# Performance work log

Measured on AMD Instinct MI355X. Metric: run time of the kernel, lower is better.

## Reference

```python
import jax, jax.numpy as jnp
import numpy as np

N_V, N_E = 4096, 16384
IN_V, OUT_V, IN_E = 128, 128, 64


def setup_inputs() -> dict:
    key = jax.random.key(0)
    k1, k2, k3, k4, k5, k6, k7 = jax.random.split(key, 7)
    stdv = 1.0 / np.sqrt(OUT_V)
    return {
        "H_v": jax.random.normal(k1, (N_V, IN_V), dtype=jnp.float32),
        "H_e": jax.random.normal(k2, (N_E, IN_E), dtype=jnp.float32),
        "adj_e": jnp.zeros((1, 1), dtype=jnp.float32),  # unused in node_layer branch
        "adj_v": jax.random.uniform(k3, (N_V, N_V), dtype=jnp.float32),
        "T": jax.random.uniform(k4, (N_V, N_E), dtype=jnp.float32),
        "weight": jax.random.uniform(k5, (IN_V, OUT_V), minval=-stdv, maxval=stdv, dtype=jnp.float32),
        "p": jax.random.normal(k6, (1, IN_E), dtype=jnp.float32),
        "bias": jax.random.uniform(k7, (OUT_V,), minval=-stdv, maxval=stdv, dtype=jnp.float32),
    }


def reference(H_v, H_e, adj_e, adj_v, T, weight, p, bias):
    # node_layer=True branch of AlternateConvolution.forward
    # diag((H_e @ p.T).T[0]) -> per-edge scalar; T @ diag(d) == column-scale T
    diag_vals = (H_e @ p.T)[:, 0]                      # [n_e]
    multiplier1 = (T * diag_vals[None, :]) @ T.T       # [n_v, n_v]
    eye = jnp.eye(multiplier1.shape[0], dtype=multiplier1.dtype)
    M1 = eye + (1.0 - eye) * multiplier1               # diagonal forced to 1
    adjusted_A = M1 * adj_v                            # elementwise adjacency mask
    ret = adjusted_A @ (H_v @ weight) + bias           # [n_v, out_v]
    return (ret, H_e)
```

## Files before the change

kernel.cpp:

```cpp
#include <hip/hip_runtime.h>
#include <stdint.h>


typedef __attribute__((ext_vector_type(4))) float floatx4;
typedef __attribute__((ext_vector_type(4))) int intx4;
typedef __attribute__((ext_vector_type(16))) int intx16;
typedef __attribute__((ext_vector_type(8))) short short8;
typedef __attribute__((ext_vector_type(4))) unsigned short u16x4;

#define AS1 __attribute__((address_space(1)))
#define AS3 __attribute__((address_space(3)))

__device__ __forceinline__ void gload_lds16(const void* g, void* l) {
  __builtin_amdgcn_global_load_lds(
      (const AS1 unsigned int*)(uintptr_t)g,
      (AS3 unsigned int*)(uint32_t)(uintptr_t)l, 16, 0, 0);
}

__device__ __forceinline__ unsigned short f32_to_bf16(float f) {
  union { float f; unsigned int u; } v;
  v.f = f;
  unsigned int r = 0x7fffu + ((v.u >> 16) & 1u);
  return (unsigned short)((v.u + r) >> 16);
}

__device__ __forceinline__ float bf16_to_f32(unsigned short s) {
  union { unsigned int u; float f; } cv;
  cv.u = (unsigned int)s << 16;
  return cv.f;
}

__device__ __forceinline__ void tri_decode(int t, int& bi, int& bj) {
  bi = 0;
  while (t >= 32 - bi) { t -= 32 - bi; ++bi; }
  bj = bi + t;
}

#define TA_SCALE 3.96875f
#define DEQ_SCALE (32.0f / 16129.0f)

__global__ __launch_bounds__(256) void edge_dot_kernel(
    const float* __restrict__ He, const float* __restrict__ p,
    float* __restrict__ dvals) {
  int e = blockIdx.x * 4 + (threadIdx.x >> 6);
  int lane = threadIdx.x & 63;
  float v = He[e * 64 + lane] * p[lane];
#pragma unroll
  for (int off = 32; off > 0; off >>= 1) v += __shfl_down(v, off);
  if (lane == 0) dvals[e] = v;
}

__global__ __launch_bounds__(256) void copy4_kernel(
    const floatx4* __restrict__ src, floatx4* __restrict__ dst, int n4) {
  int i = blockIdx.x * 256 + threadIdx.x;
  if (i < n4)
    __builtin_nontemporal_store(__builtin_nontemporal_load(src + i), dst + i);
}

__global__ __launch_bounds__(256) void convert_T_i8_kernel(
    const floatx4* __restrict__ T4, const float* __restrict__ dvals,
    uint2* __restrict__ Ta8, uint2* __restrict__ Tb8) {
  int i = blockIdx.x * 256 + threadIdx.x;
  floatx4 t0 = __builtin_nontemporal_load(T4 + 2 * i);
  floatx4 t1 = __builtin_nontemporal_load(T4 + 2 * i + 1);
  int col = (i << 3) & 16383;
  const floatx4* dv = (const floatx4*)(dvals + col);
  floatx4 d0 = dv[0], d1 = dv[1];
  union { signed char c[8]; uint2 u; } qa, qb;
#pragma unroll
  for (int q = 0; q < 4; ++q) {
    float sa0 = fminf(fmaxf(t0[q] * d0[q] * TA_SCALE, -127.f), 127.f);
    float sa1 = fminf(fmaxf(t1[q] * d1[q] * TA_SCALE, -127.f), 127.f);
    qa.c[q]     = (signed char)(int)rintf(sa0);
    qa.c[q + 4] = (signed char)(int)rintf(sa1);
    qb.c[q]     = (signed char)(int)rintf(t0[q] * 127.0f);
    qb.c[q + 4] = (signed char)(int)rintf(t1[q] * 127.0f);
  }
  Ta8[i] = qa.u;
  Tb8[i] = qb.u;
}

__global__ __launch_bounds__(256) void hwt_kernel(
    const float* __restrict__ Hv, const float* __restrict__ W,
    unsigned short* __restrict__ HWT) {
  int idx = blockIdx.x * 256 + threadIdx.x;
  int j = idx & 4095, o = idx >> 12;
  float s = 0.f;
#pragma unroll 8
  for (int c = 0; c < 128; ++c) s += Hv[j * 128 + c] * W[c * 128 + o];
  HWT[o * 4096 + j] = f32_to_bf16(s);
}

__global__ __launch_bounds__(256) void gemm1_split_kernel(
    const signed char* __restrict__ Ta, const signed char* __restrict__ Tb,
    int* __restrict__ part) {
  constexpr int K = 16384;
  __shared__ __align__(16) signed char As[2][128 * 128];
  __shared__ __align__(16) signed char Bs[2][128 * 128];

  const int d = blockIdx.x;
  const int rank = (d & 7) * 132 + (d >> 3);
  const int h = rank >= 528 ? 1 : 0;
  const int t = rank - h * 528;
  int bi, bj;
  tri_decode(t, bi, bj);

  const int tid = threadIdx.x;
  const int wave = tid >> 6, lane = tid & 63;
  const int wr = (wave >> 1) * 64, wc = (wave & 1) * 64;
  const int row32 = lane & 31, khalf = lane >> 5;

  const int srow = tid >> 3;
  const int cg = (tid & 7) ^ (srow & 7);
  const signed char* Ag = Ta + (size_t)(bi * 128 + srow) * K + cg * 16;
  const signed char* Bg = Tb + (size_t)(bj * 128 + srow) * K + cg * 16;

  intx16 acc[2][2] = {};

  const int kbeg = h * 8192, kend = kbeg + 8192;

  auto stage = [&](int b, int k0) {
#pragma unroll
    for (int q = 0; q < 4; ++q) {
      gload_lds16(Ag + (size_t)(q * 32) * K + k0, &As[b][q * 4096 + tid * 16]);
      gload_lds16(Bg + (size_t)(q * 32) * K + k0, &Bs[b][q * 4096 + tid * 16]);
    }
  };

  auto compute = [&](int b) {
    intx4 af[2][4], bf[2][4];
#pragma unroll
    for (int x = 0; x < 2; ++x) {
      const int ra = wr + x * 32 + row32;
      const int rb = wc + x * 32 + row32;
#pragma unroll
      for (int sk = 0; sk < 4; ++sk) {
        af[x][sk] =
            *(const intx4*)&As[b][ra * 128 + ((sk * 2 + khalf) ^ (ra & 7)) * 16];
        bf[x][sk] =
            *(const intx4*)&Bs[b][rb * 128 + ((sk * 2 + khalf) ^ (rb & 7)) * 16];
      }
    }
#pragma unroll
    for (int sk = 0; sk < 4; ++sk)
#pragma unroll
      for (int tr = 0; tr < 2; ++tr)
#pragma unroll
        for (int tc = 0; tc < 2; ++tc)
          acc[tr][tc] = __builtin_amdgcn_mfma_i32_32x32x32_i8(
              af[tr][sk], bf[tc][sk], acc[tr][tc], 0, 0, 0);
  };

  stage(0, kbeg);
  __syncthreads();
  int buf = 0;
  for (int k0 = kbeg; k0 < kend - 128; k0 += 128) {
    stage(buf ^ 1, k0 + 128);
    compute(buf);
    __syncthreads();
    buf ^= 1;
  }
  compute(buf);

  int* pt = part + ((size_t)h * 528 + t) * 16384;
#pragma unroll
  for (int tr = 0; tr < 2; ++tr)
#pragma unroll
    for (int tc = 0; tc < 2; ++tc) {
      const int col = wc + tc * 32 + row32;
#pragma unroll
      for (int r = 0; r < 16; ++r) {
        const int row = wr + tr * 32 + (r & 3) + 8 * (r >> 2) + 4 * khalf;
        __builtin_nontemporal_store(acc[tr][tc][r], &pt[row * 128 + col]);
      }
    }
}

__global__ __launch_bounds__(256) void combine_kernel(
    const int* __restrict__ part, const float* __restrict__ adj_v,
    unsigned short* __restrict__ adjA) {
  constexpr int NV = 4096;
  __shared__ unsigned short mt[128 * 68];

  const int b = blockIdx.x;
  const int t = b >> 1, r0 = (b & 1) * 64;
  int bi, bj;
  tri_decode(t, bi, bj);
  const int tid = threadIdx.x;
  const bool diag = (bi == bj);

  const int* pt0 = part + (size_t)t * 16384;
  const int* pt1 = pt0 + (size_t)528 * 16384;

#pragma unroll
  for (int j = 0; j < 8; ++j) {
    const int e = j * 1024 + tid * 4;
    const int row = r0 + (e >> 7);
    const int col = e & 127;
    intx4 a = __builtin_nontemporal_load((const intx4*)(pt0 + row * 128 + col));
    intx4 c = __builtin_nontemporal_load((const intx4*)(pt1 + row * 128 + col));
    floatx4 msk = __builtin_nontemporal_load(
        (const floatx4*)(adj_v + (size_t)(bi * 128 + row) * NV + bj * 128 + col));
    u16x4 o;
#pragma unroll
    for (int q = 0; q < 4; ++q) {
      float m = (float)(a[q] + c[q]) * DEQ_SCALE;
      float val = (diag && row == col + q) ? msk[q] : m * msk[q];
      ((unsigned short*)&o)[q] = f32_to_bf16(val);
      if (!diag) mt[(col + q) * 68 + (row - r0)] = f32_to_bf16(m);
    }
    *(u16x4*)(adjA + (size_t)(bi * 128 + row) * NV + bj * 128 + col) = o;
  }

  if (diag) return;
  __syncthreads();

#pragma unroll
  for (int j = 0; j < 8; ++j) {
    const int e = j * 1024 + tid * 4;
    const int mc = e >> 6;
    const int mr = e & 63;
    u16x4 mv = *(const u16x4*)&mt[mc * 68 + mr];
    floatx4 msk = __builtin_nontemporal_load(
        (const floatx4*)(adj_v + (size_t)(bj * 128 + mc) * NV + bi * 128 + r0 + mr));
    u16x4 o;
#pragma unroll
    for (int q = 0; q < 4; ++q)
      ((unsigned short*)&o)[q] =
          f32_to_bf16(bf16_to_f32(((const unsigned short*)&mv)[q]) * msk[q]);
    *(u16x4*)(adjA + (size_t)(bj * 128 + mc) * NV + bi * 128 + r0 + mr) = o;
  }
}

__global__ __launch_bounds__(256) void gemm2_kernel(
    const unsigned short* __restrict__ adjA, const unsigned short* __restrict__ HWT,
    float* __restrict__ gpart) {
  constexpr int K = 4096, OUTV = 128;
  __shared__ __align__(16) unsigned short As[2][128 * 32];
  __shared__ __align__(16) unsigned short Bs[2][128 * 32];

  const int tid = threadIdx.x;
  const int wave = tid >> 6, lane = tid & 63;
  const int bi = blockIdx.x, ks = blockIdx.y;
  const int wr = (wave >> 1) * 64, wc = (wave & 1) * 64;
  const int quad = lane >> 4, mrow = lane & 15;

  const int sr = tid >> 2, sc = (tid & 3) * 8;
  const unsigned short* Ag = adjA + (size_t)(bi * 128 + sr) * K + sc;
  const unsigned short* Bg = HWT + (size_t)sr * K + sc;

  floatx4 acc[4][4] = {};

  const int kbeg = ks * 512, kend = kbeg + 512;

  auto stage = [&](int b, int k0) {
    gload_lds16(Ag + k0, &As[b][tid * 8]);
    gload_lds16(Ag + (size_t)64 * K + k0, &As[b][tid * 8 + 2048]);
    gload_lds16(Bg + k0, &Bs[b][tid * 8]);
    gload_lds16(Bg + (size_t)64 * K + k0, &Bs[b][tid * 8 + 2048]);
  };

  auto compute = [&](int b) {
    short8 af[4], bf[4];
#pragma unroll
    for (int x = 0; x < 4; ++x) {
      af[x] = *(const short8*)&As[b][(wr + x * 16 + mrow) * 32 + quad * 8];
      bf[x] = *(const short8*)&Bs[b][(wc + x * 16 + mrow) * 32 + quad * 8];
    }
#pragma unroll
    for (int tr = 0; tr < 4; ++tr)
#pragma unroll
      for (int tc = 0; tc < 4; ++tc)
        acc[tr][tc] = __builtin_amdgcn_mfma_f32_16x16x32_bf16(
            af[tr], bf[tc], acc[tr][tc], 0, 0, 0);
  };

  stage(0, kbeg);
  __syncthreads();
  int buf = 0;
  for (int k0 = kbeg; k0 < kend - 32; k0 += 32) {
    stage(buf ^ 1, k0 + 32);
    compute(buf);
    __syncthreads();
    buf ^= 1;
  }
  compute(buf);

#pragma unroll
  for (int tr = 0; tr < 4; ++tr) {
    const int rbase = bi * 128 + wr + tr * 16 + quad * 4;
#pragma unroll
    for (int tc = 0; tc < 4; ++tc) {
      const int col = wc + tc * 16 + mrow;
#pragma unroll
      for (int r = 0; r < 4; ++r)
        gpart[(size_t)ks * 524288 + (size_t)(rbase + r) * OUTV + col] =
            acc[tr][tc][r];
    }
  }
}

__global__ __launch_bounds__(256) void reduce_bias_kernel(
    const float* __restrict__ gpart, const float* __restrict__ bias,
    float* __restrict__ out) {
  int i = blockIdx.x * 256 + threadIdx.x;
  floatx4 acc = *(const floatx4*)&bias[(i & 31) * 4];
#pragma unroll
  for (int ks = 0; ks < 8; ++ks)
    acc += __builtin_nontemporal_load((const floatx4*)gpart +
                                      (size_t)ks * 131072 + i);
  __builtin_nontemporal_store(acc, (floatx4*)out + i);
}

extern "C" void kernel_launch(void* const* d_in, const int* in_sizes, int n_in,
                              void* d_out, int out_size, void* d_ws, size_t ws_size,
                              hipStream_t stream) {
  const float* H_v    = (const float*)d_in[0];
  const float* H_e    = (const float*)d_in[1];
  const float* adj_v  = (const float*)d_in[3];
  const float* T      = (const float*)d_in[4];
  const float* weight = (const float*)d_in[5];
  const float* p      = (const float*)d_in[6];
  const float* bias   = (const float*)d_in[7];
  float* out = (float*)d_out;

  char* ws = (char*)d_ws;
  signed char* Ta      = (signed char*)(ws);
  signed char* Tb      = (signed char*)(ws + 67108864);
  int* part            = (int*)(ws + 134217728);
  unsigned short* adjA = (unsigned short*)(ws + 203423744);
  unsigned short* HWT  = (unsigned short*)(ws + 236978176);
  float* dvals         = (float*)(ws + 238026752);
  float* gpart         = (float*)(ws + 238092288);

  edge_dot_kernel<<<dim3(4096), dim3(256), 0, stream>>>(H_e, p, dvals);
  copy4_kernel<<<dim3(1024), dim3(256), 0, stream>>>(
      (const floatx4*)H_e, (floatx4*)(out + 524288), 262144);
  hwt_kernel<<<dim3(2048), dim3(256), 0, stream>>>(H_v, weight, HWT);

  convert_T_i8_kernel<<<dim3(32768), dim3(256), 0, stream>>>(
      (const floatx4*)T, dvals, (uint2*)Ta, (uint2*)Tb);

  gemm1_split_kernel<<<dim3(1056), dim3(256), 0, stream>>>(Ta, Tb, part);
  combine_kernel<<<dim3(1056), dim3(256), 0, stream>>>(part, adj_v, adjA);

  gemm2_kernel<<<dim3(32, 8), dim3(256), 0, stream>>>(adjA, HWT, gpart);
  reduce_bias_kernel<<<dim3(512), dim3(256), 0, stream>>>(gpart, bias, out);
}
```

Baseline: 663.0 us.

## Tile H_v@W through LDS and issue next-stage loads after fragment reads

The H_v@W kernel now loads all of W and a 32-row slab of H_v into shared memory, and each thread computes 16 outputs with vector FMAs. This replaces one thread per output re-reading global memory, and the grid drops from 2048 to 128 blocks. In both GEMM loops the prefetch of the next K tile is now issued after the current fragments are read into registers and before the MFMAs, folding the last iteration into the loop with a guard. The goal is better overlap of async global-to-LDS loads with matrix math. The cost is 64KB+ of LDS per block in the H_v@W kernel, which limits occupancy.

```diff
diff --git a/kernel.cpp b/kernel.cpp
--- a/kernel.cpp
+++ b/kernel.cpp
@@ -83,12 +83,35 @@
 __global__ __launch_bounds__(256) void hwt_kernel(
     const float* __restrict__ Hv, const float* __restrict__ W,
     unsigned short* __restrict__ HWT) {
-  int idx = blockIdx.x * 256 + threadIdx.x;
-  int j = idx & 4095, o = idx >> 12;
-  float s = 0.f;
-#pragma unroll 8
-  for (int c = 0; c < 128; ++c) s += Hv[j * 128 + c] * W[c * 128 + o];
-  HWT[o * 4096 + j] = f32_to_bf16(s);
+  __shared__ float Ws[128 * 128];
+  __shared__ float Hs[32 * 132];
+  const int tid = threadIdx.x;
+#pragma unroll
+  for (int i = 0; i < 16; ++i) {
+    const int g = i * 1024 + tid * 4;
+    *(floatx4*)&Ws[g] = *(const floatx4*)&W[g];
+  }
+  const int j0 = blockIdx.x * 32;
+#pragma unroll
+  for (int i = 0; i < 4; ++i) {
+    const int g = i * 1024 + tid * 4;
+    *(floatx4*)&Hs[(g >> 7) * 132 + (g & 127)] =
+        *(const floatx4*)&Hv[j0 * 128 + g];
+  }
+  __syncthreads();
+  const int j = tid >> 3, l7 = tid & 7;
+  floatx4 acc[4] = {};
+  for (int c = 0; c < 128; ++c) {
+    const float h = Hs[j * 132 + c];
+#pragma unroll
+    for (int m = 0; m < 4; ++m)
+      acc[m] += h * *(const floatx4*)&Ws[c * 128 + m * 32 + l7 * 4];
+  }
+#pragma unroll
+  for (int m = 0; m < 4; ++m)
+#pragma unroll
+    for (int r = 0; r < 4; ++r)
+      HWT[(size_t)(m * 32 + l7 * 4 + r) * 4096 + j0 + j] = f32_to_bf16(acc[m][r]);
 }
 
 __global__ __launch_bounds__(256) void gemm1_split_kernel(
@@ -127,7 +150,10 @@
     }
   };
 
-  auto compute = [&](int b) {
+  stage(0, kbeg);
+  __syncthreads();
+  int buf = 0;
+  for (int k0 = kbeg; k0 < kend; k0 += 128) {
     intx4 af[2][4], bf[2][4];
 #pragma unroll
     for (int x = 0; x < 2; ++x) {
@@ -136,11 +162,12 @@
 #pragma unroll
       for (int sk = 0; sk < 4; ++sk) {
         af[x][sk] =
-            *(const intx4*)&As[b][ra * 128 + ((sk * 2 + khalf) ^ (ra & 7)) * 16];
+            *(const intx4*)&As[buf][ra * 128 + ((sk * 2 + khalf) ^ (ra & 7)) * 16];
         bf[x][sk] =
-            *(const intx4*)&Bs[b][rb * 128 + ((sk * 2 + khalf) ^ (rb & 7)) * 16];
+            *(const intx4*)&Bs[buf][rb * 128 + ((sk * 2 + khalf) ^ (rb & 7)) * 16];
       }
     }
+    if (k0 + 128 < kend) stage(buf ^ 1, k0 + 128);
 #pragma unroll
     for (int sk = 0; sk < 4; ++sk)
 #pragma unroll
@@ -149,18 +176,9 @@
         for (int tc = 0; tc < 2; ++tc)
           acc[tr][tc] = __builtin_amdgcn_mfma_i32_32x32x32_i8(
               af[tr][sk], bf[tc][sk], acc[tr][tc], 0, 0, 0);
-  };
-
-  stage(0, kbeg);
-  __syncthreads();
-  int buf = 0;
-  for (int k0 = kbeg; k0 < kend - 128; k0 += 128) {
-    stage(buf ^ 1, k0 + 128);
-    compute(buf);
     __syncthreads();
     buf ^= 1;
   }
-  compute(buf);
 
   int* pt = part + ((size_t)h * 528 + t) * 16384;
 #pragma unroll
@@ -260,31 +278,26 @@
     gload_lds16(Bg + (size_t)64 * K + k0, &Bs[b][tid * 8 + 2048]);
   };
 
-  auto compute = [&](int b) {
+  stage(0, kbeg);
+  __syncthreads();
+  int buf = 0;
+  for (int k0 = kbeg; k0 < kend; k0 += 32) {
     short8 af[4], bf[4];
 #pragma unroll
     for (int x = 0; x < 4; ++x) {
-      af[x] = *(const short8*)&As[b][(wr + x * 16 + mrow) * 32 + quad * 8];
-      bf[x] = *(const short8*)&Bs[b][(wc + x * 16 + mrow) * 32 + quad * 8];
-    }
+      af[x] = *(const short8*)&As[buf][(wr + x * 16 + mrow) * 32 + quad * 8];
+      bf[x] = *(const short8*)&Bs[buf][(wc + x * 16 + mrow) * 32 + quad * 8];
+    }
+    if (k0 + 32 < kend) stage(buf ^ 1, k0 + 32);
 #pragma unroll
     for (int tr = 0; tr < 4; ++tr)
 #pragma unroll
       for (int tc = 0; tc < 4; ++tc)
         acc[tr][tc] = __builtin_amdgcn_mfma_f32_16x16x32_bf16(
             af[tr], bf[tc], acc[tr][tc], 0, 0, 0);
-  };
-
-  stage(0, kbeg);
-  __syncthreads();
-  int buf = 0;
-  for (int k0 = kbeg; k0 < kend - 32; k0 += 32) {
-    stage(buf ^ 1, k0 + 32);
-    compute(buf);
     __syncthreads();
     buf ^= 1;
   }
-  compute(buf);
 
 #pragma unroll
   for (int tr = 0; tr < 4; ++tr) {
@@ -336,7 +349,7 @@
   edge_dot_kernel<<<dim3(4096), dim3(256), 0, stream>>>(H_e, p, dvals);
   copy4_kernel<<<dim3(1024), dim3(256), 0, stream>>>(
       (const floatx4*)H_e, (floatx4*)(out + 524288), 262144);
-  hwt_kernel<<<dim3(2048), dim3(256), 0, stream>>>(H_v, weight, HWT);
+  hwt_kernel<<<dim3(128), dim3(256), 0, stream>>>(H_v, weight, HWT);
 
   convert_T_i8_kernel<<<dim3(32768), dim3(256), 0, stream>>>(
       (const floatx4*)T, dvals, (uint2*)Ta, (uint2*)Tb);
```

Result: no change. 664.1 us (+0.2%).
